# Optimization experiments

Hardware: AMD Instinct MI355X
Metric: run time of the kernel (lower is better)

The kernel has to match this reference:

```python
import jax, jax.numpy as jnp
import numpy as np

H, NH, HD = 1024, 16, 64
B, T, S = 2, 1024, 3
NOISE, STEP, TEMP, NSTEPS = 0.1, 0.01, 1.0, 5
LN_EPS = 1e-5


def setup_inputs() -> dict:
    key = jax.random.key(0)
    ks = jax.random.split(key, 9)
    return {
        "queries": jax.random.normal(ks[0], (B, NH, T, HD), jnp.float32),
        "keys": jax.random.normal(ks[1], (B, NH, T, HD), jnp.float32),
        "values": jax.random.normal(ks[2], (B, NH, T, HD), jnp.float32),
        "hidden_states": jax.random.normal(ks[3], (B, T, H), jnp.float32),
        "W1": jax.random.normal(ks[4], (H, H), jnp.float32) * 0.02,
        "b1": jnp.zeros((H,), jnp.float32),
        "ln_g": jnp.ones((H,), jnp.float32),
        "ln_b": jnp.zeros((H,), jnp.float32),
        "W2": jax.random.normal(ks[5], (H, H), jnp.float32) * 0.02,
        "b2": jnp.zeros((H,), jnp.float32),
        "hyp_noise": jax.random.normal(ks[6], (S, B, NH, T, HD), jnp.float32),
        "ref_noise": jax.random.normal(ks[7], (S, NSTEPS - 1, B, NH, T, HD), jnp.float32),
    }


def _attention_energy(q, k, v):
    # q: [S,B,H,T,D]; k,v: [B,H,T,D] -> energy [S,B]
    scores = jnp.einsum('sbhtd,bhud->sbhtu', q, k) / jnp.sqrt(jnp.float32(q.shape[-1]))
    attn = jax.nn.softmax(scores, axis=-1)
    out = jnp.einsum('sbhtu,bhud->sbhtd', attn, v)
    out_mag = jnp.linalg.norm(out, axis=-1).mean(axis=(2, 3))          # [S,B]
    entropy = -(attn * jnp.log(attn + 1e-8)).sum(axis=-1).mean(axis=(2, 3))
    align = (q * k[None]).sum(axis=-1).mean(axis=(2, 3))
    return out_mag - 0.1 * entropy - 0.05 * align


def reference(queries, keys, values, hidden_states, W1, b1, ln_g, ln_b, W2, b2,
              hyp_noise, ref_noise):
    # query_predictor: Linear -> LayerNorm -> ReLU -> Linear
    x = hidden_states @ W1.T + b1
    mu = x.mean(axis=-1, keepdims=True)
    var = ((x - mu) ** 2).mean(axis=-1, keepdims=True)
    x = (x - mu) / jnp.sqrt(var + LN_EPS) * ln_g + ln_b
    x = jax.nn.relu(x)
    ctx = x @ W2.T + b2                                   # [B,T,H]
    ctx = ctx.reshape(B, T, NH, HD).transpose(0, 2, 1, 3) # [B,NH,T,HD]

    # exploration hypotheses, refined jointly over the sample axis
    q = queries[None] + hyp_noise * NOISE                 # [S,B,NH,T,HD]
    for step in range(NSTEPS):
        q = q - STEP * (q - ctx[None])                    # PCN prediction-error update
        if step < NSTEPS - 1:
            q = q + ref_noise[:, step] * 0.01

    energies = _attention_energy(q, keys, values)         # [S,B]
    probs = jax.nn.softmax(-energies / TEMP, axis=0)      # [S,B]
    selected = jnp.einsum('sb,sbhtd->bhtd', probs, q)     # softmax-weighted mix
    return selected, keys, values
```

## Files before the change

### kernel.cpp

```cpp
#include <hip/hip_runtime.h>
#include <hip/hip_bf16.h>
#include <math.h>

#define NB 2
#define NHH 16
#define TT 1024
#define HDD 64
#define NSS 3
#define HH 1024

typedef float f4 __attribute__((ext_vector_type(4)));
typedef short bf16x8 __attribute__((ext_vector_type(8)));
typedef unsigned short u16;
typedef u16 u16x4 __attribute__((ext_vector_type(4)));

__device__ inline u16 f2bf(float f) {
    union { float f; unsigned u; } v; v.f = f;
    unsigned r = (v.u + 0x7FFFu + ((v.u >> 16) & 1u)) >> 16;
    return (u16)r;
}
__device__ inline float bf2f(u16 u) {
    union { unsigned u; float f; } v; v.u = ((unsigned)u) << 16;
    return v.f;
}
__device__ inline unsigned cvtpk(float lo, float hi) {
    unsigned r;
    asm("v_cvt_pk_bf16_f32 %0, %1, %2" : "=v"(r) : "v"(lo), "v"(hi));
    return r;
}
__device__ inline void gl_lds16(const u16* g, u16* l) {
    __builtin_amdgcn_global_load_lds(
        (const __attribute__((address_space(1))) unsigned int*)g,
        (__attribute__((address_space(3))) unsigned int*)l, 16, 0, 0);
}

__device__ inline float red16sum(float v) {
    v += __shfl_xor(v, 1);
    v += __shfl_xor(v, 2);
    v += __shfl_xor(v, 4);
    v += __shfl_xor(v, 8);
    return v;
}
__device__ inline float red64sum(float v) {
    v += __shfl_xor(v, 1);
    v += __shfl_xor(v, 2);
    v += __shfl_xor(v, 4);
    v += __shfl_xor(v, 8);
    v += __shfl_xor(v, 16);
    v += __shfl_xor(v, 32);
    return v;
}

#define PCN_CH 0.0950990050f
#define PCN_C0 0.0096059601f
#define PCN_C1 0.0097029900f
#define PCN_C2 0.0098010000f
#define PCN_C3 0.0099000000f

__global__ __launch_bounds__(256) void k_prep(const float* __restrict__ hyp,
                                              const float* __restrict__ rn,
                                              u16* __restrict__ noise16,
                                              const float* __restrict__ hs, u16* __restrict__ hs_b,
                                              const float* __restrict__ W1, u16* __restrict__ w1_b,
                                              const float* __restrict__ W2, u16* __restrict__ w2_b,
                                              const float* __restrict__ keys, u16* __restrict__ k_b,
                                              float* __restrict__ outk,
                                              const float* __restrict__ V, u16* __restrict__ vt_b,
                                              float* __restrict__ outv) {
    __shared__ float tile[64][65];
    int b = blockIdx.x;
    if (b < 1536) {
        int sidx = b >> 9, blk = b & 511;
        size_t so = (size_t)sidx * 2097152;
        int o = blk * 4096 + threadIdx.x * 4;
        const float* hp = hyp + so;
        const float* r0 = rn + (size_t)(sidx * 4 + 0) * 2097152;
        const float* r1 = rn + (size_t)(sidx * 4 + 1) * 2097152;
        const float* r2 = rn + (size_t)(sidx * 4 + 2) * 2097152;
        const float* r3 = rn + (size_t)(sidx * 4 + 3) * 2097152;
        u16* np = noise16 + so;
        f4 vh[4], v0[4], v1[4], v2[4], v3[4];
#pragma unroll
        for (int j = 0; j < 4; ++j) {
            vh[j] = __builtin_nontemporal_load((const f4*)(hp + o + j * 1024));
            v0[j] = __builtin_nontemporal_load((const f4*)(r0 + o + j * 1024));
            v1[j] = __builtin_nontemporal_load((const f4*)(r1 + o + j * 1024));
            v2[j] = __builtin_nontemporal_load((const f4*)(r2 + o + j * 1024));
            v3[j] = __builtin_nontemporal_load((const f4*)(r3 + o + j * 1024));
        }
#pragma unroll
        for (int j = 0; j < 4; ++j) {
            f4 v = PCN_CH * vh[j] + PCN_C0 * v0[j] + PCN_C1 * v1[j] +
                   PCN_C2 * v2[j] + PCN_C3 * v3[j];
            unsigned pr[2];
            pr[0] = cvtpk(v[0], v[1]);
            pr[1] = cvtpk(v[2], v[3]);
            *(uint2*)(np + o + j * 1024) = *(uint2*)pr;
        }
        return;
    }
    if (b < 5632) {
        int b2 = b - 1536;
        const float* s; u16* d; int base;
        if (b2 < 2048)      { s = hs; d = hs_b; base = 0; }
        else if (b2 < 3072) { s = W1; d = w1_b; base = 2048; }
        else                { s = W2; d = w2_b; base = 3072; }
        int i = (b2 - base) * 256 + threadIdx.x;
        f4 v = ((const f4*)s)[i];
        u16x4 o;
        o[0] = f2bf(v[0]); o[1] = f2bf(v[1]); o[2] = f2bf(v[2]); o[3] = f2bf(v[3]);
        ((u16x4*)d)[i] = o;
        return;
    }
    if (b < 6656) {
        int c = (b - 5632) * 256 + threadIdx.x;
        int bh = c >> 13, t = (c >> 3) & 1023, col8 = c & 7;
        int kt = t >> 6, row = t & 63;
        const float* sp = keys + (size_t)c * 8;
        f4 v0 = *(const f4*)(sp);
        f4 v1 = *(const f4*)(sp + 4);
        *(f4*)(outk + (size_t)c * 8) = v0;
        *(f4*)(outk + (size_t)c * 8 + 4) = v1;
        union { unsigned u[4]; int4 i4; } o;
        o.u[0] = cvtpk(v0[0] * 0.125f, v0[1] * 0.125f);
        o.u[1] = cvtpk(v0[2] * 0.125f, v0[3] * 0.125f);
        o.u[2] = cvtpk(v1[0] * 0.125f, v1[1] * 0.125f);
        o.u[3] = cvtpk(v1[2] * 0.125f, v1[3] * 0.125f);
        *(int4*)(k_b + (size_t)(bh * 16 + kt) * 4096 + row * 64 + ((col8 ^ (row & 7)) << 3)) = o.i4;
        return;
    }
    int idx = b - 6656;
    int bh = idx >> 4, kt = idx & 15, t0 = kt * 64;
    int r = threadIdx.x >> 2, c0 = (threadIdx.x & 3) * 16;
    const float* vp = V + ((size_t)bh * TT + t0) * HDD;
#pragma unroll
    for (int j = 0; j < 16; j += 4) {
        f4 v = *(const f4*)(vp + r * HDD + c0 + j);
        tile[r][c0 + j + 0] = v[0]; tile[r][c0 + j + 1] = v[1];
        tile[r][c0 + j + 2] = v[2]; tile[r][c0 + j + 3] = v[3];
        *(f4*)(outv + ((size_t)bh * TT + t0 + r) * HDD + c0 + j) = v;
    }
    __syncthreads();
    int d = threadIdx.x >> 2, x0 = (threadIdx.x & 3) * 16;
    u16* op = vt_b + (size_t)(bh * 16 + kt) * 4096 + d * 64;
#pragma unroll
    for (int cc = 0; cc < 2; ++cc) {
        int c8 = (x0 >> 3) + cc;
        union { unsigned u[4]; int4 i4; } o;
#pragma unroll
        for (int p = 0; p < 4; ++p)
            o.u[p] = cvtpk(tile[c8 * 8 + 2 * p][d], tile[c8 * 8 + 2 * p + 1][d]);
        *(int4*)(op + ((c8 ^ (d & 7)) << 3)) = o.i4;
    }
}

template <int EPI>
__global__ __launch_bounds__(256) void k_gemm_bt(const u16* __restrict__ A,
                                                 const u16* __restrict__ Bm,
                                                 const float* __restrict__ bias,
                                                 const float* __restrict__ que,
                                                 void* __restrict__ outv) {
    const int K = 1024, N = 1024;
    int w = threadIdx.x >> 6, l = threadIdx.x & 63, lr = l & 15, lg = l >> 4;
    int m0 = blockIdx.y * 64 + w * 16;
    int n0 = blockIdx.x * 64;
    const u16* ap = A + (size_t)(m0 + lr) * K + lg * 8;
    const u16* bp = Bm + (size_t)(n0 + lr) * K + lg * 8;
    f4 z4 = {0.f, 0.f, 0.f, 0.f};
    f4 acc[4] = {z4, z4, z4, z4};
#pragma unroll 2
    for (int kk = 0; kk < K; kk += 32) {
        bf16x8 a  = *(const bf16x8*)(ap + kk);
        bf16x8 b0 = *(const bf16x8*)(bp + kk);
        bf16x8 b1 = *(const bf16x8*)(bp + 16 * K + kk);
        bf16x8 b2 = *(const bf16x8*)(bp + 32 * K + kk);
        bf16x8 b3 = *(const bf16x8*)(bp + 48 * K + kk);
        acc[0] = __builtin_amdgcn_mfma_f32_16x16x32_bf16(a, b0, acc[0], 0, 0, 0);
        acc[1] = __builtin_amdgcn_mfma_f32_16x16x32_bf16(a, b1, acc[1], 0, 0, 0);
        acc[2] = __builtin_amdgcn_mfma_f32_16x16x32_bf16(a, b2, acc[2], 0, 0, 0);
        acc[3] = __builtin_amdgcn_mfma_f32_16x16x32_bf16(a, b3, acc[3], 0, 0, 0);
    }
    const float A5 = 0.9509900499f, CC = 1.0f - A5;
#pragma unroll
    for (int cf = 0; cf < 4; ++cf) {
        int col = n0 + cf * 16 + lr;
        float bs = bias[col];
#pragma unroll
        for (int r = 0; r < 4; ++r) {
            int row = m0 + lg * 4 + r;
            float v = acc[cf][r] + bs;
            if (EPI == 0) {
                ((u16*)outv)[(size_t)row * N + col] = f2bf(v);
            } else {
                int b = row >> 10, t = row & 1023, nh = col >> 6, hd = col & 63;
                size_t oidx = (((size_t)(b * NHH + nh)) * TT + t) * HDD + hd;
                ((float*)outv)[oidx] = A5 * que[oidx] + CC * v;
            }
        }
    }
}

__global__ __launch_bounds__(256) void k_lnrelu(const u16* __restrict__ X,
                                                const float* __restrict__ g,
                                                const float* __restrict__ bta,
                                                u16* __restrict__ xr) {
    int row = blockIdx.x;
    u16x4 xv = ((const u16x4*)(X + (size_t)row * HH))[threadIdx.x];
    f4 v;
    v[0] = bf2f(xv[0]); v[1] = bf2f(xv[1]); v[2] = bf2f(xv[2]); v[3] = bf2f(xv[3]);
    float s = v[0] + v[1] + v[2] + v[3];
    float s2 = v[0] * v[0] + v[1] * v[1] + v[2] * v[2] + v[3] * v[3];
    s = red64sum(s);
    s2 = red64sum(s2);
    __shared__ float red[8];
    int w = threadIdx.x >> 6, l = threadIdx.x & 63;
    if (l == 0) { red[w] = s; red[w + 4] = s2; }
    __syncthreads();
    float S1 = red[0] + red[1] + red[2] + red[3];
    float S2 = red[4] + red[5] + red[6] + red[7];
    float mu = S1 * (1.0f / 1024.0f);
    float var = S2 * (1.0f / 1024.0f) - mu * mu;
    float rstd = rsqrtf(var + 1e-5f);
    f4 gv = ((const f4*)g)[threadIdx.x];
    f4 bv = ((const f4*)bta)[threadIdx.x];
    u16x4 o;
#pragma unroll
    for (int j = 0; j < 4; ++j) {
        float y = (v[j] - mu) * rstd * gv[j] + bv[j];
        y = fmaxf(y, 0.f);
        o[j] = f2bf(y);
    }
    ((u16x4*)(xr + (size_t)row * HH))[threadIdx.x] = o;
}

__global__ __launch_bounds__(256, 3) void k_attn(const float* __restrict__ basep_,
                                                 const u16* __restrict__ noise16,
                                                 const u16* __restrict__ Kb,
                                                 const u16* __restrict__ Vt,
                                                 float* __restrict__ part) {
    int bi = blockIdx.x;
    int p_ = bi & 31, j_ = bi >> 5;
    int h = p_ & 15, b = p_ >> 4;
    int s = j_ >> 3, qt2 = j_ & 7;
    int sb = s * 2 + b;
    int bh = b * NHH + h;
    int pi = sb * 128 + h * 8 + qt2;
    int w = threadIdx.x >> 6, l = threadIdx.x & 63, lr = l & 15, lg = l >> 4;
    int t0 = qt2 * 128;
    f4 z4 = {0.f, 0.f, 0.f, 0.f};

    __shared__ u16 Ks[2][4096];
    __shared__ u16 Vs[2][4096];
    __shared__ u16 plds[8][1024];

    const u16* kT = Kb + (size_t)(bh * 16) * 4096;
    const u16* vT = Vt + (size_t)(bh * 16) * 4096;

#pragma unroll
    for (int j = 0; j < 2; ++j) {
        int co = (w + 4 * j) * 512;
        gl_lds16(kT + co + l * 8, &Ks[0][co]);
        gl_lds16(vT + co + l * 8, &Vs[0][co]);
    }

    const float* basep = basep_ + (size_t)bh * TT * HDD;
    const u16* noisep = noise16 + (size_t)s * 2097152 + (size_t)bh * TT * HDD;

    char* slab = (char*)&plds[0][0];
    {
        int t = threadIdx.x;
#pragma unroll
        for (int m = 0; m < 4; ++m) {
            int j = t + 256 * m;
            size_t off = (size_t)t0 * HDD + (size_t)j * 8;
            f4 a0 = *(const f4*)(basep + off);
            f4 a1 = *(const f4*)(basep + off + 4);
            union { int4 i4; u16 u[8]; } nv;
            nv.i4 = *(const int4*)(noisep + off);
#pragma unroll
            for (int k = 0; k < 4; ++k) {
                a0[k] += bf2f(nv.u[k]);
                a1[k] += bf2f(nv.u[4 + k]);
            }
            union { unsigned u[4]; int4 i4; } o;
            o.u[0] = cvtpk(a0[0], a0[1]); o.u[1] = cvtpk(a0[2], a0[3]);
            o.u[2] = cvtpk(a1[0], a1[1]); o.u[3] = cvtpk(a1[2], a1[3]);
            int row = j >> 3, slot = j & 7;
            *(int4*)(slab + row * 128 + (((slot ^ (row & 7))) << 4)) = o.i4;
        }
    }
    __syncthreads();

    bf16x8 aq[2][2];
#pragma unroll
    for (int qr = 0; qr < 2; ++qr) {
        int r_ = w * 32 + qr * 16 + lr;
#pragma unroll
        for (int c = 0; c < 2; ++c)
            aq[qr][c] = *(const bf16x8*)(slab + r_ * 128 + (((c * 4 + lg) ^ (r_ & 7)) << 4));
    }

    f4 acco[2][4] = {{z4, z4, z4, z4}, {z4, z4, z4, z4}};
    float zrow[2][4] = {{0.f, 0.f, 0.f, 0.f}, {0.f, 0.f, 0.f, 0.f}};
    float wrow[2][4] = {{0.f, 0.f, 0.f, 0.f}, {0.f, 0.f, 0.f, 0.f}};
    float al_lane = 0.f;
    int kdiag = qt2 * 2 + (w >> 1);

    for (int kt = 0; kt < 16; ++kt) {
        int cur = kt & 1;
        if (kt < 15) {
#pragma unroll
            for (int j = 0; j < 2; ++j) {
                int co = (w + 4 * j) * 512;
                gl_lds16(kT + (kt + 1) * 4096 + co + l * 8, &Ks[cur ^ 1][co]);
                gl_lds16(vT + (kt + 1) * 4096 + co + l * 8, &Vs[cur ^ 1][co]);
            }
        }
        char* KsB = (char*)Ks[cur];
        char* VsB = (char*)Vs[cur];

        f4 sc[2][4];
        __builtin_amdgcn_s_setprio(1);
#pragma unroll
        for (int cf = 0; cf < 4; ++cf) {
            int row = cf * 16 + lr, rs = row & 7;
            bf16x8 bk0 = *(const bf16x8*)(KsB + row * 128 + ((lg ^ rs) << 4));
            bf16x8 bk1 = *(const bf16x8*)(KsB + row * 128 + (((4 + lg) ^ rs) << 4));
            f4 t0a = __builtin_amdgcn_mfma_f32_16x16x32_bf16(aq[0][0], bk0, z4, 0, 0, 0);
            sc[0][cf] = __builtin_amdgcn_mfma_f32_16x16x32_bf16(aq[0][1], bk1, t0a, 0, 0, 0);
            f4 t1a = __builtin_amdgcn_mfma_f32_16x16x32_bf16(aq[1][0], bk0, z4, 0, 0, 0);
            sc[1][cf] = __builtin_amdgcn_mfma_f32_16x16x32_bf16(aq[1][1], bk1, t1a, 0, 0, 0);
        }
        __builtin_amdgcn_s_setprio(0);

        if (kt == kdiag) {
            f4 sd0 = (w & 1) ? sc[0][2] : sc[0][0];
            f4 sd1 = (w & 1) ? sc[1][3] : sc[1][1];
            int rr = lr & 3;
            float e0 = rr == 0 ? sd0[0] : (rr == 1 ? sd0[1] : (rr == 2 ? sd0[2] : sd0[3]));
            float e1 = rr == 0 ? sd1[0] : (rr == 1 ? sd1[1] : (rr == 2 ? sd1[2] : sd1[3]));
            if (lg == (lr >> 2)) al_lane += (e0 + e1) * 8.0f;
        }

#pragma unroll
        for (int qr = 0; qr < 2; ++qr) {
            u16* pl = &plds[w * 2 + qr][0];
#pragma unroll
            for (int cf = 0; cf < 4; ++cf) {
                float p0 = __expf(sc[qr][cf][0]);
                float p1 = __expf(sc[qr][cf][1]);
                float p2 = __expf(sc[qr][cf][2]);
                float p3 = __expf(sc[qr][cf][3]);
                zrow[qr][0] += p0; zrow[qr][1] += p1;
                zrow[qr][2] += p2; zrow[qr][3] += p3;
                wrow[qr][0] = fmaf(p0, sc[qr][cf][0], wrow[qr][0]);
                wrow[qr][1] = fmaf(p1, sc[qr][cf][1], wrow[qr][1]);
                wrow[qr][2] = fmaf(p2, sc[qr][cf][2], wrow[qr][2]);
                wrow[qr][3] = fmaf(p3, sc[qr][cf][3], wrow[qr][3]);
                unsigned pa01 = cvtpk(p0, p1), pa23 = cvtpk(p2, p3);
                int base_ = cf * 16 + lr;
                pl[(((lg * 4 + 0) * 64 + base_)) ^ (((lg * 4 + 0) & 7) << 3)] = (u16)pa01;
                pl[(((lg * 4 + 1) * 64 + base_)) ^ (((lg * 4 + 1) & 7) << 3)] = (u16)(pa01 >> 16);
                pl[(((lg * 4 + 2) * 64 + base_)) ^ (((lg * 4 + 2) & 7) << 3)] = (u16)pa23;
                pl[(((lg * 4 + 3) * 64 + base_)) ^ (((lg * 4 + 3) & 7) << 3)] = (u16)(pa23 >> 16);
            }
        }
        bf16x8 pa[2][2];
#pragma unroll
        for (int qr = 0; qr < 2; ++qr) {
            const u16* pl = &plds[w * 2 + qr][0];
            pa[qr][0] = *(const bf16x8*)&pl[(lr * 64 + lg * 8) ^ ((lr & 7) << 3)];
            pa[qr][1] = *(const bf16x8*)&pl[(lr * 64 + 32 + lg * 8) ^ ((lr & 7) << 3)];
        }
        __builtin_amdgcn_s_setprio(1);
#pragma unroll
        for (int cf = 0; cf < 4; ++cf) {
            int row = cf * 16 + lr, rs = row & 7;
            bf16x8 bv0 = *(const bf16x8*)(VsB + row * 128 + ((lg ^ rs) << 4));
            bf16x8 bv1 = *(const bf16x8*)(VsB + row * 128 + (((4 + lg) ^ rs) << 4));
            acco[0][cf] = __builtin_amdgcn_mfma_f32_16x16x32_bf16(pa[0][0], bv0, acco[0][cf], 0, 0, 0);
            acco[0][cf] = __builtin_amdgcn_mfma_f32_16x16x32_bf16(pa[0][1], bv1, acco[0][cf], 0, 0, 0);
            acco[1][cf] = __builtin_amdgcn_mfma_f32_16x16x32_bf16(pa[1][0], bv0, acco[1][cf], 0, 0, 0);
            acco[1][cf] = __builtin_amdgcn_mfma_f32_16x16x32_bf16(pa[1][1], bv1, acco[1][cf], 0, 0, 0);
        }
        __builtin_amdgcn_s_setprio(0);

        __syncthreads();
    }

    float magw = 0.f, entw = 0.f;
#pragma unroll
    for (int qr = 0; qr < 2; ++qr) {
#pragma unroll
        for (int r = 0; r < 4; ++r) {
            float zz = red16sum(zrow[qr][r]);
            float ww = red16sum(wrow[qr][r]);
            float ssq = acco[qr][0][r] * acco[qr][0][r] + acco[qr][1][r] * acco[qr][1][r] +
                        acco[qr][2][r] * acco[qr][2][r] + acco[qr][3][r] * acco[qr][3][r];
            ssq = red16sum(ssq);
            float inv = 1.0f / zz;
            magw += sqrtf(ssq) * inv;
            entw += __logf(zz) - ww * inv;
        }
    }
    magw += __shfl_xor(magw, 16); magw += __shfl_xor(magw, 32);
    entw += __shfl_xor(entw, 16); entw += __shfl_xor(entw, 32);
    float al = red64sum(al_lane);

    __shared__ float red[4][3];
    if (l == 0) { red[w][0] = magw; red[w][1] = entw; red[w][2] = al; }
    __syncthreads();
    if (threadIdx.x == 0) {
        part[pi * 3 + 0] = red[0][0] + red[1][0] + red[2][0] + red[3][0];
        part[pi * 3 + 1] = red[0][1] + red[1][1] + red[2][1] + red[3][1];
        part[pi * 3 + 2] = red[0][2] + red[1][2] + red[2][2] + red[3][2];
    }
}

__global__ void k_finalize(const float* __restrict__ part, float* __restrict__ probs) {
    int w = threadIdx.x >> 6, l = threadIdx.x & 63;
    __shared__ float eng[6];
    if (w < 6) {
        float a0 = 0.f, a1 = 0.f, a2 = 0.f;
        for (int i = l; i < 128; i += 64) {
            const float* pp = part + (size_t)(w * 128 + i) * 3;
            a0 += pp[0]; a1 += pp[1]; a2 += pp[2];
        }
        a0 = red64sum(a0); a1 = red64sum(a1); a2 = red64sum(a2);
        if (l == 0) {
            const float inv = 1.0f / 16384.0f;
            eng[w] = a0 * inv - 0.1f * (a1 * inv) - 0.05f * (a2 * inv);
        }
    }
    __syncthreads();
    if (threadIdx.x < 2) {
        int b = threadIdx.x;
        float e0 = -eng[0 + b], e1 = -eng[2 + b], e2 = -eng[4 + b];
        float mx = fmaxf(e0, fmaxf(e1, e2));
        float x0 = __expf(e0 - mx), x1 = __expf(e1 - mx), x2 = __expf(e2 - mx);
        float inv = 1.0f / (x0 + x1 + x2);
        probs[0 + b] = x0 * inv;
        probs[2 + b] = x1 * inv;
        probs[4 + b] = x2 * inv;
    }
}

__global__ __launch_bounds__(256) void k_select(const float* __restrict__ base,
                                                const u16* __restrict__ noise16,
                                                const float* __restrict__ probs,
                                                float* __restrict__ out) {
    const int NG = 524288;
    int i = blockIdx.x * 256 + threadIdx.x;
    int b = i >> 18;
    float p0 = probs[0 + b], p1 = probs[2 + b], p2 = probs[4 + b];
    f4 v = ((const f4*)base)[i];
    u16x4 n0 = ((const u16x4*)noise16)[i];
    u16x4 n1 = ((const u16x4*)noise16)[NG + i];
    u16x4 n2 = ((const u16x4*)noise16)[2 * NG + i];
#pragma unroll
    for (int j = 0; j < 4; ++j)
        v[j] += p0 * bf2f(n0[j]) + p1 * bf2f(n1[j]) + p2 * bf2f(n2[j]);
    ((f4*)out)[i] = v;
}

extern "C" void kernel_launch(void* const* d_in, const int* in_sizes, int n_in,
                              void* d_out, int out_size, void* d_ws, size_t ws_size,
                              hipStream_t stream) {
    const float* queries = (const float*)d_in[0];
    const float* keys    = (const float*)d_in[1];
    const float* values  = (const float*)d_in[2];
    const float* hs      = (const float*)d_in[3];
    const float* W1      = (const float*)d_in[4];
    const float* b1      = (const float*)d_in[5];
    const float* ln_g    = (const float*)d_in[6];
    const float* ln_b    = (const float*)d_in[7];
    const float* W2      = (const float*)d_in[8];
    const float* b2      = (const float*)d_in[9];
    const float* hyp     = (const float*)d_in[10];
    const float* rn      = (const float*)d_in[11];
    float* out = (float*)d_out;
    char* ws = (char*)d_ws;

    const size_t MB = 1024ull * 1024ull;
    u16*   hs_b  = (u16*)(ws + 0 * MB);
    u16*   w1_b  = (u16*)(ws + 4 * MB);
    u16*   w2_b  = (u16*)(ws + 6 * MB);
    u16*   X     = (u16*)(ws + 8 * MB);
    u16*   xr    = (u16*)(ws + 12 * MB);
    u16*   n16   = (u16*)(ws + 16 * MB);
    float* base  = (float*)(ws + 28 * MB);
    u16*   k_b   = (u16*)(ws + 36 * MB);
    u16*   vt_b  = (u16*)(ws + 40 * MB);
    float* part  = (float*)(ws + 44 * MB);
    float* probs = (float*)(ws + 44 * MB + 65536);

    k_prep<<<7168, 256, 0, stream>>>(hyp, rn, n16,
                                     hs, hs_b, W1, w1_b, W2, w2_b,
                                     keys, k_b, out + 2097152,
                                     values, vt_b, out + 4194304);

    k_gemm_bt<0><<<dim3(16, 32), 256, 0, stream>>>(hs_b, w1_b, b1, nullptr, X);
    k_lnrelu<<<2048, 256, 0, stream>>>(X, ln_g, ln_b, xr);
    k_gemm_bt<1><<<dim3(16, 32), 256, 0, stream>>>(xr, w2_b, b2, queries, base);

    k_attn<<<768, 256, 0, stream>>>(base, n16, k_b, vt_b, part);
    k_finalize<<<1, 384, 0, stream>>>(part, probs);
    k_select<<<2048, 256, 0, stream>>>(base, n16, probs, out);
}
```

Baseline: 169.6 us.

## Fuse finalize into attention via last-block counter; use exp2 scores; widen select

Removes the separate single-block finalize launch by having the last finishing attention block, detected with an atomic counter that the prep kernel resets, reduce the partials and compute the sample probabilities. Pre-scales K by log2(e) so the softmax can use exp2f, and corrects the entropy and alignment terms by ln2. Also switches the noise-prep loads from nontemporal to normal loads and has each select thread process two vectors with half the blocks. The trade-offs are an extra atomic plus threadfence per attention block and a serialized tail reduction on one block.

```diff
diff --git a/kernel.cpp b/kernel.cpp
--- a/kernel.cpp
+++ b/kernel.cpp
@@ -13,6 +13,9 @@
 typedef short bf16x8 __attribute__((ext_vector_type(8)));
 typedef unsigned short u16;
 typedef u16 u16x4 __attribute__((ext_vector_type(4)));
+
+#define LOG2E 1.4426950408889634f
+#define LN2   0.6931471805599453f
 
 __device__ inline u16 f2bf(float f) {
     union { float f; unsigned u; } v; v.f = f;
@@ -66,9 +69,11 @@
                                               const float* __restrict__ keys, u16* __restrict__ k_b,
                                               float* __restrict__ outk,
                                               const float* __restrict__ V, u16* __restrict__ vt_b,
-                                              float* __restrict__ outv) {
+                                              float* __restrict__ outv,
+                                              int* __restrict__ cnt) {
     __shared__ float tile[64][65];
     int b = blockIdx.x;
+    if (b == 0 && threadIdx.x == 0) *cnt = 0;
     if (b < 1536) {
         int sidx = b >> 9, blk = b & 511;
         size_t so = (size_t)sidx * 2097152;
@@ -82,11 +87,11 @@
         f4 vh[4], v0[4], v1[4], v2[4], v3[4];
 #pragma unroll
         for (int j = 0; j < 4; ++j) {
-            vh[j] = __builtin_nontemporal_load((const f4*)(hp + o + j * 1024));
-            v0[j] = __builtin_nontemporal_load((const f4*)(r0 + o + j * 1024));
-            v1[j] = __builtin_nontemporal_load((const f4*)(r1 + o + j * 1024));
-            v2[j] = __builtin_nontemporal_load((const f4*)(r2 + o + j * 1024));
-            v3[j] = __builtin_nontemporal_load((const f4*)(r3 + o + j * 1024));
+            vh[j] = *(const f4*)(hp + o + j * 1024);
+            v0[j] = *(const f4*)(r0 + o + j * 1024);
+            v1[j] = *(const f4*)(r1 + o + j * 1024);
+            v2[j] = *(const f4*)(r2 + o + j * 1024);
+            v3[j] = *(const f4*)(r3 + o + j * 1024);
         }
 #pragma unroll
         for (int j = 0; j < 4; ++j) {
@@ -113,6 +118,7 @@
         return;
     }
     if (b < 6656) {
+        const float SC = 0.125f * LOG2E;
         int c = (b - 5632) * 256 + threadIdx.x;
         int bh = c >> 13, t = (c >> 3) & 1023, col8 = c & 7;
         int kt = t >> 6, row = t & 63;
@@ -122,10 +128,10 @@
         *(f4*)(outk + (size_t)c * 8) = v0;
         *(f4*)(outk + (size_t)c * 8 + 4) = v1;
         union { unsigned u[4]; int4 i4; } o;
-        o.u[0] = cvtpk(v0[0] * 0.125f, v0[1] * 0.125f);
-        o.u[1] = cvtpk(v0[2] * 0.125f, v0[3] * 0.125f);
-        o.u[2] = cvtpk(v1[0] * 0.125f, v1[1] * 0.125f);
-        o.u[3] = cvtpk(v1[2] * 0.125f, v1[3] * 0.125f);
+        o.u[0] = cvtpk(v0[0] * SC, v0[1] * SC);
+        o.u[1] = cvtpk(v0[2] * SC, v0[3] * SC);
+        o.u[2] = cvtpk(v1[0] * SC, v1[1] * SC);
+        o.u[3] = cvtpk(v1[2] * SC, v1[3] * SC);
         *(int4*)(k_b + (size_t)(bh * 16 + kt) * 4096 + row * 64 + ((col8 ^ (row & 7)) << 3)) = o.i4;
         return;
     }
@@ -237,7 +243,9 @@
                                                  const u16* __restrict__ noise16,
                                                  const u16* __restrict__ Kb,
                                                  const u16* __restrict__ Vt,
-                                                 float* __restrict__ part) {
+                                                 float* __restrict__ part,
+                                                 float* __restrict__ probs,
+                                                 int* __restrict__ cnt) {
     int bi = blockIdx.x;
     int p_ = bi & 31, j_ = bi >> 5;
     int h = p_ & 15, b = p_ >> 4;
@@ -339,7 +347,7 @@
             int rr = lr & 3;
             float e0 = rr == 0 ? sd0[0] : (rr == 1 ? sd0[1] : (rr == 2 ? sd0[2] : sd0[3]));
             float e1 = rr == 0 ? sd1[0] : (rr == 1 ? sd1[1] : (rr == 2 ? sd1[2] : sd1[3]));
-            if (lg == (lr >> 2)) al_lane += (e0 + e1) * 8.0f;
+            if (lg == (lr >> 2)) al_lane += (e0 + e1) * (8.0f * LN2);
         }
 
 #pragma unroll
@@ -347,10 +355,10 @@
             u16* pl = &plds[w * 2 + qr][0];
 #pragma unroll
             for (int cf = 0; cf < 4; ++cf) {
-                float p0 = __expf(sc[qr][cf][0]);
-                float p1 = __expf(sc[qr][cf][1]);
-                float p2 = __expf(sc[qr][cf][2]);
-                float p3 = __expf(sc[qr][cf][3]);
+                float p0 = exp2f(sc[qr][cf][0]);
+                float p1 = exp2f(sc[qr][cf][1]);
+                float p2 = exp2f(sc[qr][cf][2]);
+                float p3 = exp2f(sc[qr][cf][3]);
                 zrow[qr][0] += p0; zrow[qr][1] += p1;
                 zrow[qr][2] += p2; zrow[qr][3] += p3;
                 wrow[qr][0] = fmaf(p0, sc[qr][cf][0], wrow[qr][0]);
@@ -400,7 +408,7 @@
             ssq = red16sum(ssq);
             float inv = 1.0f / zz;
             magw += sqrtf(ssq) * inv;
-            entw += __logf(zz) - ww * inv;
+            entw += __logf(zz) - (ww * LN2) * inv;
         }
     }
     magw += __shfl_xor(magw, 16); magw += __shfl_xor(magw, 32);
@@ -408,40 +416,48 @@
     float al = red64sum(al_lane);
 
     __shared__ float red[4][3];
+    __shared__ int lastdone;
     if (l == 0) { red[w][0] = magw; red[w][1] = entw; red[w][2] = al; }
     __syncthreads();
     if (threadIdx.x == 0) {
         part[pi * 3 + 0] = red[0][0] + red[1][0] + red[2][0] + red[3][0];
         part[pi * 3 + 1] = red[0][1] + red[1][1] + red[2][1] + red[3][1];
         part[pi * 3 + 2] = red[0][2] + red[1][2] + red[2][2] + red[3][2];
-    }
-}
-
-__global__ void k_finalize(const float* __restrict__ part, float* __restrict__ probs) {
-    int w = threadIdx.x >> 6, l = threadIdx.x & 63;
+        __threadfence();
+        lastdone = (atomicAdd(cnt, 1) == 767);
+    }
+    __syncthreads();
+    if (!lastdone) return;
+
+    __threadfence();
+    volatile const float* pv = part;
     __shared__ float eng[6];
-    if (w < 6) {
+#pragma unroll
+    for (int pass = 0; pass < 2; ++pass) {
+        int e = pass == 0 ? w : 4 + w;
+        if (pass == 1 && w >= 2) break;
         float a0 = 0.f, a1 = 0.f, a2 = 0.f;
         for (int i = l; i < 128; i += 64) {
-            const float* pp = part + (size_t)(w * 128 + i) * 3;
-            a0 += pp[0]; a1 += pp[1]; a2 += pp[2];
+            a0 += pv[(e * 128 + i) * 3 + 0];
+            a1 += pv[(e * 128 + i) * 3 + 1];
+            a2 += pv[(e * 128 + i) * 3 + 2];
         }
         a0 = red64sum(a0); a1 = red64sum(a1); a2 = red64sum(a2);
         if (l == 0) {
             const float inv = 1.0f / 16384.0f;
-            eng[w] = a0 * inv - 0.1f * (a1 * inv) - 0.05f * (a2 * inv);
+            eng[e] = a0 * inv - 0.1f * (a1 * inv) - 0.05f * (a2 * inv);
         }
     }
     __syncthreads();
     if (threadIdx.x < 2) {
-        int b = threadIdx.x;
-        float e0 = -eng[0 + b], e1 = -eng[2 + b], e2 = -eng[4 + b];
+        int bb = threadIdx.x;
+        float e0 = -eng[0 + bb], e1 = -eng[2 + bb], e2 = -eng[4 + bb];
         float mx = fmaxf(e0, fmaxf(e1, e2));
         float x0 = __expf(e0 - mx), x1 = __expf(e1 - mx), x2 = __expf(e2 - mx);
         float inv = 1.0f / (x0 + x1 + x2);
-        probs[0 + b] = x0 * inv;
-        probs[2 + b] = x1 * inv;
-        probs[4 + b] = x2 * inv;
+        probs[0 + bb] = x0 * inv;
+        probs[2 + bb] = x1 * inv;
+        probs[4 + bb] = x2 * inv;
     }
 }
 
@@ -450,17 +466,21 @@
                                                 const float* __restrict__ probs,
                                                 float* __restrict__ out) {
     const int NG = 524288;
-    int i = blockIdx.x * 256 + threadIdx.x;
-    int b = i >> 18;
+    int i0 = (blockIdx.x * 256 + threadIdx.x) * 2;
+    int b = i0 >> 18;
     float p0 = probs[0 + b], p1 = probs[2 + b], p2 = probs[4 + b];
-    f4 v = ((const f4*)base)[i];
-    u16x4 n0 = ((const u16x4*)noise16)[i];
-    u16x4 n1 = ((const u16x4*)noise16)[NG + i];
-    u16x4 n2 = ((const u16x4*)noise16)[2 * NG + i];
-#pragma unroll
-    for (int j = 0; j < 4; ++j)
-        v[j] += p0 * bf2f(n0[j]) + p1 * bf2f(n1[j]) + p2 * bf2f(n2[j]);
-    ((f4*)out)[i] = v;
+#pragma unroll
+    for (int j = 0; j < 2; ++j) {
+        int i = i0 + j;
+        f4 v = ((const f4*)base)[i];
+        u16x4 n0 = ((const u16x4*)noise16)[i];
+        u16x4 n1 = ((const u16x4*)noise16)[NG + i];
+        u16x4 n2 = ((const u16x4*)noise16)[2 * NG + i];
+#pragma unroll
+        for (int k = 0; k < 4; ++k)
+            v[k] += p0 * bf2f(n0[k]) + p1 * bf2f(n1[k]) + p2 * bf2f(n2[k]);
+        ((f4*)out)[i] = v;
+    }
 }
 
 extern "C" void kernel_launch(void* const* d_in, const int* in_sizes, int n_in,
@@ -493,17 +513,17 @@
     u16*   vt_b  = (u16*)(ws + 40 * MB);
     float* part  = (float*)(ws + 44 * MB);
     float* probs = (float*)(ws + 44 * MB + 65536);
+    int*   cnt   = (int*)(ws + 44 * MB + 131072);
 
     k_prep<<<7168, 256, 0, stream>>>(hyp, rn, n16,
                                      hs, hs_b, W1, w1_b, W2, w2_b,
                                      keys, k_b, out + 2097152,
-                                     values, vt_b, out + 4194304);
+                                     values, vt_b, out + 4194304, cnt);
 
     k_gemm_bt<0><<<dim3(16, 32), 256, 0, stream>>>(hs_b, w1_b, b1, nullptr, X);
     k_lnrelu<<<2048, 256, 0, stream>>>(X, ln_g, ln_b, xr);
     k_gemm_bt<1><<<dim3(16, 32), 256, 0, stream>>>(xr, w2_b, b2, queries, base);
 
-    k_attn<<<768, 256, 0, stream>>>(base, n16, k_b, vt_b, part);
-    k_finalize<<<1, 384, 0, stream>>>(part, probs);
-    k_select<<<2048, 256, 0, stream>>>(base, n16, probs, out);
-}
+    k_attn<<<768, 256, 0, stream>>>(base, n16, k_b, vt_b, part, probs, cnt);
+    k_select<<<1024, 256, 0, stream>>>(base, n16, probs, out);
+}
```

Result: slower. 184.5 us (+8.8%).
